# Kernel optimization log

Measured on AMD Instinct MI355X. Metric: run time of the kernel, lower is better.

## Reference

```python
import jax, jax.numpy as jnp
import numpy as np
import math

B_SZ, L, D_MODEL = 2, 2048, 1024
D_STATE, D_CONV, EXPAND = 16, 4, 2
D_INNER = EXPAND * D_MODEL
DT_RANK = math.ceil(D_MODEL / 16)


def setup_inputs() -> dict:
    key = jax.random.key(0)
    ks = jax.random.split(key, 9)
    s = 0.02
    x = jax.random.normal(ks[0], (B_SZ, L, D_MODEL), jnp.float32)
    W_in = jax.random.normal(ks[1], (D_MODEL, 2 * D_INNER), jnp.float32) * s
    conv_w = jax.random.normal(ks[2], (D_INNER, D_CONV), jnp.float32) * 0.1
    conv_b = jax.random.normal(ks[3], (D_INNER,), jnp.float32) * s
    W_xproj = jax.random.normal(ks[4], (D_INNER, DT_RANK + 2 * D_STATE), jnp.float32) * s
    W_dt = jax.random.normal(ks[5], (DT_RANK, D_INNER), jnp.float32) * s
    # dt bias init so softplus(bias) is log-uniform in [dt_min, dt_max]
    dt_min, dt_max = 0.001, 0.1
    dt = jnp.exp(jax.random.uniform(ks[6], (D_INNER,)) * (math.log(dt_max) - math.log(dt_min)) + math.log(dt_min))
    dt = jnp.maximum(dt, 1e-4)
    b_dt = dt + jnp.log(-jnp.expm1(-dt))
    A_log = jnp.log(jnp.broadcast_to(jnp.arange(1, D_STATE + 1, dtype=jnp.float32), (D_INNER, D_STATE)))
    D = jnp.ones((D_INNER,), jnp.float32)
    W_out = jax.random.normal(ks[7], (D_INNER, D_MODEL), jnp.float32) * s
    return {"x": x, "W_in": W_in, "conv_w": conv_w, "conv_b": conv_b,
            "W_xproj": W_xproj, "W_dt": W_dt, "b_dt": b_dt,
            "A_log": A_log, "D": D, "W_out": W_out}


def _silu(v):
    return v * jax.nn.sigmoid(v)


def _mamba_fwd(x, W_in, conv_w, conv_b, W_xproj, W_dt, b_dt, A_log, D, W_out):
    B, Ls, _ = x.shape
    xz = x @ W_in                         # (B, L, 2*d_inner)
    xb, z = jnp.split(xz, 2, axis=-1)
    # causal depthwise conv1d (pad left d_conv-1, truncate to L)
    xp = jnp.pad(xb, ((0, 0), (D_CONV - 1, 0), (0, 0)))
    conv = conv_b
    acc = jnp.zeros_like(xb)
    for k in range(D_CONV):
        acc = acc + xp[:, k:k + Ls, :] * conv_w[:, k]
    xb = _silu(acc + conv_b)
    # input-dependent dt, B, C
    proj = xb @ W_xproj                   # (B, L, dt_rank + 2*d_state)
    dt_in = proj[..., :DT_RANK]
    Bm = proj[..., DT_RANK:DT_RANK + D_STATE]   # (B, L, d_state)
    Cm = proj[..., DT_RANK + D_STATE:]          # (B, L, d_state)
    dt = jax.nn.softplus(dt_in @ W_dt + b_dt)   # (B, L, d_inner)
    A = -jnp.exp(A_log)                         # (d_inner, d_state)

    def step(h, inp):
        x_t, dt_t, B_t, C_t = inp               # (B,d_inner),(B,d_inner),(B,s),(B,s)
        dA = jnp.exp(dt_t[:, :, None] * A)      # (B, d_inner, d_state)
        h = dA * h + (dt_t[:, :, None] * B_t[:, None, :]) * x_t[:, :, None]
        y_t = jnp.einsum('bds,bs->bd', h, C_t)
        return h, y_t

    h0 = jnp.zeros((B, D_INNER, D_STATE), xb.dtype)
    xs = (xb.swapaxes(0, 1), dt.swapaxes(0, 1), Bm.swapaxes(0, 1), Cm.swapaxes(0, 1))
    _, ys = jax.lax.scan(step, h0, xs)          # (L, B, d_inner)
    y = ys.swapaxes(0, 1) + D * xb
    y = y * _silu(z)
    return y @ W_out                            # (B, L, d_model)


def reference(x, W_in, conv_w, conv_b, W_xproj, W_dt, b_dt, A_log, D, W_out):
    return _mamba_fwd(x, W_in, conv_w, conv_b, W_xproj, W_dt, b_dt, A_log, D, W_out)
```

## Files before the change

kernel.cpp:

```cpp
#include <hip/hip_runtime.h>
#include <hip/hip_bf16.h>
#include <math.h>

#define BSZ 2
#define LSEQ 2048
#define DMODEL 1024
#define DSTATE 16
#define DCONV 4
#define DINNER 2048
#define DTRANK 64
#define NPROJ (DTRANK + 2 * DSTATE)
#define NC 32
#define LC 64
#define KS 4
#define KCH (DINNER / KS)
#define TT 8

using short8 = __attribute__((ext_vector_type(8))) short;
using f32x4 = __attribute__((ext_vector_type(4))) float;
using u16x4 = __attribute__((ext_vector_type(4))) unsigned short;

__device__ __forceinline__ float silu_f(float v) {
    return v / (1.f + expf(-v));
}
__device__ __forceinline__ float softplus_f(float v) {
    return fmaxf(v, 0.f) + log1pf(expf(-fabsf(v)));
}
__device__ __forceinline__ unsigned short f2bf(float f) {
    unsigned u = __builtin_bit_cast(unsigned, f);
    u += 0x7fffu + ((u >> 16) & 1u);
    return (unsigned short)(u >> 16);
}
__device__ __forceinline__ float bf2f(unsigned short u) {
    unsigned x = ((unsigned)u) << 16;
    return __builtin_bit_cast(float, x);
}

__device__ __forceinline__ void gld_lds16(const unsigned short* g, unsigned short* l) {
    __builtin_amdgcn_global_load_lds(
        (const __attribute__((address_space(1))) unsigned int*)g,
        (__attribute__((address_space(3))) unsigned int*)l, 16, 0, 0);
}

__device__ __forceinline__ int xcd_swz(int wg, int nwg) {
    return (wg & 7) * (nwg >> 3) + (wg >> 3);
}

__global__ __launch_bounds__(256) void f32_to_bf16_kernel(
    const float* __restrict__ in, unsigned short* __restrict__ out, int n4) {
    int i = blockIdx.x * 256 + threadIdx.x;
    if (i >= n4) return;
    float4 v = reinterpret_cast<const float4*>(in)[i];
    u16x4 o = {f2bf(v.x), f2bf(v.y), f2bf(v.z), f2bf(v.w)};
    reinterpret_cast<u16x4*>(out)[i] = o;
}

__global__ __launch_bounds__(256) void transpose_bf16_kernel(
    const float* __restrict__ in, unsigned short* __restrict__ out, int R, int Cc) {
    __shared__ float t[32][33];
    const int tx = threadIdx.x & 31, ty = threadIdx.x >> 5;
    const int c0 = blockIdx.x * 32, r0 = blockIdx.y * 32;
    for (int i = ty; i < 32; i += 8)
        t[i][tx] = in[(size_t)(r0 + i) * Cc + c0 + tx];
    __syncthreads();
    for (int i = ty; i < 32; i += 8)
        out[(size_t)(c0 + i) * R + r0 + tx] = f2bf(t[tx][i]);
}

template <int EPI, typename CT>
__global__ __launch_bounds__(512) void gemm256(
    const unsigned short* __restrict__ A, const unsigned short* __restrict__ Bt,
    CT* __restrict__ C, CT* __restrict__ C2, int M, int N, int K) {
    extern __shared__ __align__(16) unsigned short lds[];
    unsigned short* As = lds;
    unsigned short* Bs = lds + 3 * 8192;
    const int tid = threadIdx.x;
    const int lane = tid & 63;
    const int w = tid >> 6;
    const int wm = w >> 2, wn = w & 3;
    const int nwg = gridDim.x * gridDim.y;
    const int wg = xcd_swz(blockIdx.y * gridDim.x + blockIdx.x, nwg);
    const int m0 = (wg / gridDim.x) * 256, n0 = (wg % gridDim.x) * 256;
    const int fr = lane & 15, kg = lane >> 4;
    const int kswz = ((kg ^ ((fr >> 1) & 3)) << 3);
    const int srow = tid >> 2;
    const int cs8 = (((tid & 3) ^ ((tid >> 3) & 3)) << 3);
    const int dst = tid * 8;
    const int nt = K / 32;

    f32x4 acc[8][4];
#pragma unroll
    for (int m = 0; m < 8; m++)
#pragma unroll
        for (int n = 0; n < 4; n++) acc[m][n] = (f32x4){0.f, 0.f, 0.f, 0.f};

#define STAGE_A(t)                                                               \
    {                                                                            \
        const int _b = (t) % 3, _k = (t) * 32;                                   \
        gld_lds16(&A[(size_t)(m0 + srow) * K + _k + cs8], &As[_b * 8192 + dst]); \
        gld_lds16(&A[(size_t)(m0 + 128 + srow) * K + _k + cs8],                  \
                  &As[_b * 8192 + dst + 4096]);                                  \
    }
#define STAGE_B(t)                                                               \
    {                                                                            \
        const int _b = (t) % 3, _k = (t) * 32;                                   \
        gld_lds16(&Bt[(size_t)(n0 + srow) * K + _k + cs8], &Bs[_b * 8192 + dst]);\
        gld_lds16(&Bt[(size_t)(n0 + 128 + srow) * K + _k + cs8],                 \
                  &Bs[_b * 8192 + dst + 4096]);                                  \
    }

    STAGE_A(0); STAGE_B(0); STAGE_A(1); STAGE_B(1);
    asm volatile("s_waitcnt vmcnt(4)" ::: "memory");
    __builtin_amdgcn_s_barrier();

    short8 bfr[4];
    for (int t = 0; t < nt; t++) {
        const int buf = t % 3;
        short8 afr[4];
#pragma unroll
        for (int q = 0; q < 4; q++)
            afr[q] = *reinterpret_cast<const short8*>(
                &As[buf * 8192 + (wm * 128 + q * 16 + fr) * 32 + kswz]);
#pragma unroll
        for (int q = 0; q < 4; q++)
            bfr[q] = *reinterpret_cast<const short8*>(
                &Bs[buf * 8192 + (wn * 64 + q * 16 + fr) * 32 + kswz]);
        if (t + 2 < nt) STAGE_A(t + 2);
        __builtin_amdgcn_s_barrier();
        asm volatile("s_waitcnt lgkmcnt(0)" ::: "memory");
        __builtin_amdgcn_sched_barrier(0);
        __builtin_amdgcn_s_setprio(1);
#pragma unroll
        for (int m = 0; m < 4; m++)
#pragma unroll
            for (int n = 0; n < 4; n++)
                acc[m][n] = __builtin_amdgcn_mfma_f32_16x16x32_bf16(
                    afr[m], bfr[n], acc[m][n], 0, 0, 0);
        __builtin_amdgcn_s_setprio(0);
        __builtin_amdgcn_s_barrier();
#pragma unroll
        for (int q = 0; q < 4; q++)
            afr[q] = *reinterpret_cast<const short8*>(
                &As[buf * 8192 + (wm * 128 + 64 + q * 16 + fr) * 32 + kswz]);
        if (t + 2 < nt) STAGE_B(t + 2);
        if (t + 1 < nt) {
            if (t + 2 < nt)
                asm volatile("s_waitcnt vmcnt(4)" ::: "memory");
            else
                asm volatile("s_waitcnt vmcnt(0)" ::: "memory");
        }
        __builtin_amdgcn_s_barrier();
        asm volatile("s_waitcnt lgkmcnt(0)" ::: "memory");
        __builtin_amdgcn_sched_barrier(0);
        __builtin_amdgcn_s_setprio(1);
#pragma unroll
        for (int m = 0; m < 4; m++)
#pragma unroll
            for (int n = 0; n < 4; n++)
                acc[4 + m][n] = __builtin_amdgcn_mfma_f32_16x16x32_bf16(
                    afr[m], bfr[n], acc[4 + m][n], 0, 0, 0);
        __builtin_amdgcn_s_setprio(0);
        __builtin_amdgcn_s_barrier();
    }
#undef STAGE_A
#undef STAGE_B

    const int g4 = kg * 4;
#pragma unroll
    for (int m = 0; m < 8; m++)
#pragma unroll
        for (int n = 0; n < 4; n++)
#pragma unroll
            for (int j = 0; j < 4; j++) {
                int mm = m0 + wm * 128 + m * 16 + g4 + j;
                int nn = n0 + wn * 64 + n * 16 + fr;
                float v = acc[m][n][j];
                if (EPI == 1) {
                    if (nn < DINNER)
                        C[(size_t)mm * DINNER + nn] = f2bf(v);
                    else
                        C2[(size_t)mm * DINNER + (nn - DINNER)] = f2bf(silu_f(v));
                } else {
                    if constexpr (sizeof(CT) == 2)
                        C[(size_t)mm * N + nn] = f2bf(v);
                    else
                        C[(size_t)mm * N + nn] = v;
                }
            }
}

template <int EPI, typename CT>
__global__ __launch_bounds__(256) void gemm_mfma(
    const unsigned short* __restrict__ A, const unsigned short* __restrict__ Bt,
    CT* __restrict__ C, int M, int N, int K) {
    __shared__ __align__(16) unsigned short As[2][4096];
    __shared__ __align__(16) unsigned short Bs[2][4096];
    const int tid = threadIdx.x;
    const int lane = tid & 63;
    const int wid = tid >> 6;
    const int wr = wid >> 1, wc = wid & 1;
    const int nwg = gridDim.x * gridDim.y;
    const int wg = xcd_swz(blockIdx.y * gridDim.x + blockIdx.x, nwg);
    const int m0 = (wg / gridDim.x) * 128, n0 = (wg % gridDim.x) * 128;

    const int r0 = tid >> 2;
    const int r1 = r0 + 64;
    const int d0 = tid * 8;
    const int d1 = d0 + 2048;
    const int cs8 = (((tid & 3) ^ ((tid >> 3) & 3)) << 3);

    f32x4 acc[4][4];
#pragma unroll
    for (int m = 0; m < 4; m++)
#pragma unroll
        for (int n = 0; n < 4; n++) acc[m][n] = (f32x4){0.f, 0.f, 0.f, 0.f};

    const int fr = lane & 15;
    const int kg = lane >> 4;
    const int kswz = ((kg ^ ((fr >> 1) & 3)) << 3);
    const int nt = K / 32;

    gld_lds16(&A[(size_t)(m0 + r0) * K + cs8], &As[0][d0]);
    gld_lds16(&A[(size_t)(m0 + r1) * K + cs8], &As[0][d1]);
    gld_lds16(&Bt[(size_t)(n0 + r0) * K + cs8], &Bs[0][d0]);
    gld_lds16(&Bt[(size_t)(n0 + r1) * K + cs8], &Bs[0][d1]);
    __syncthreads();

    int cur = 0;
    for (int t = 0; t < nt; t++) {
        if (t + 1 < nt) {
            const int k0 = (t + 1) * 32;
            gld_lds16(&A[(size_t)(m0 + r0) * K + k0 + cs8], &As[cur ^ 1][d0]);
            gld_lds16(&A[(size_t)(m0 + r1) * K + k0 + cs8], &As[cur ^ 1][d1]);
            gld_lds16(&Bt[(size_t)(n0 + r0) * K + k0 + cs8], &Bs[cur ^ 1][d0]);
            gld_lds16(&Bt[(size_t)(n0 + r1) * K + k0 + cs8], &Bs[cur ^ 1][d1]);
        }
        short8 a[4], b[4];
#pragma unroll
        for (int m = 0; m < 4; m++)
            a[m] = *reinterpret_cast<const short8*>(
                &As[cur][(wr * 64 + m * 16 + fr) * 32 + kswz]);
#pragma unroll
        for (int n = 0; n < 4; n++)
            b[n] = *reinterpret_cast<const short8*>(
                &Bs[cur][(wc * 64 + n * 16 + fr) * 32 + kswz]);
#pragma unroll
        for (int m = 0; m < 4; m++)
#pragma unroll
            for (int n = 0; n < 4; n++)
                acc[m][n] = __builtin_amdgcn_mfma_f32_16x16x32_bf16(
                    a[m], b[n], acc[m][n], 0, 0, 0);
        __syncthreads();
        cur ^= 1;
    }

    const int g4 = (lane >> 4) * 4;
#pragma unroll
    for (int m = 0; m < 4; m++)
#pragma unroll
        for (int n = 0; n < 4; n++)
#pragma unroll
            for (int j = 0; j < 4; j++) {
                int mm = m0 + wr * 64 + m * 16 + g4 + j;
                int nn = n0 + wc * 64 + n * 16 + fr;
                float v = acc[m][n][j];
                if constexpr (sizeof(CT) == 2)
                    C[(size_t)mm * N + nn] = f2bf(v);
                else
                    C[(size_t)mm * N + nn] = v;
            }
}

__global__ __launch_bounds__(256) void dt_gemm(
    const unsigned short* __restrict__ dtin,
    const unsigned short* __restrict__ WdtT,
    const float* __restrict__ bias,
    unsigned short* __restrict__ dtout) {
    const int lane = threadIdx.x & 63;
    const int wid = threadIdx.x >> 6;
    const int mt = wid >> 1, nh = wid & 1;
    const int m0 = blockIdx.x * 32;
    const int n0 = blockIdx.y * 128 + nh * 64;
    const int fr = lane & 15, kg = lane >> 4;

    f32x4 acc[4];
#pragma unroll
    for (int i = 0; i < 4; i++) acc[i] = (f32x4){0.f, 0.f, 0.f, 0.f};

#pragma unroll
    for (int step = 0; step < 2; step++) {
        short8 a = *reinterpret_cast<const short8*>(
            &dtin[(size_t)(m0 + mt * 16 + fr) * DTRANK + step * 32 + kg * 8]);
#pragma unroll
        for (int nt = 0; nt < 4; nt++) {
            short8 b = *reinterpret_cast<const short8*>(
                &WdtT[(size_t)(n0 + nt * 16 + fr) * DTRANK + step * 32 + kg * 8]);
            acc[nt] = __builtin_amdgcn_mfma_f32_16x16x32_bf16(a, b, acc[nt], 0, 0, 0);
        }
    }
    const int g4 = kg * 4;
#pragma unroll
    for (int nt = 0; nt < 4; nt++)
#pragma unroll
        for (int j = 0; j < 4; j++) {
            int m = m0 + mt * 16 + g4 + j;
            int n = n0 + nt * 16 + fr;
            dtout[(size_t)m * DINNER + n] = f2bf(softplus_f(acc[nt][j] + bias[n]));
        }
}

__global__ __launch_bounds__(256) void proj_splitk(
    const unsigned short* __restrict__ Abf,
    const unsigned short* __restrict__ WxT,
    float* __restrict__ pp) {
    const int lane = threadIdx.x & 63;
    const int wid = threadIdx.x >> 6;
    const int mt = wid >> 1;
    const int nh = wid & 1;
    const int m0 = blockIdx.x * 32;
    const int kc = blockIdx.y;
    const int fr = lane & 15;
    const int kg = lane >> 4;

    const size_t abase = (size_t)(m0 + mt * 16 + fr) * DINNER + kc * KCH + kg * 8;

    f32x4 acc[3];
#pragma unroll
    for (int i = 0; i < 3; i++) acc[i] = (f32x4){0.f, 0.f, 0.f, 0.f};

    for (int step = 0; step < KCH / 32; step++) {
        short8 a = *reinterpret_cast<const short8*>(&Abf[abase + step * 32]);
#pragma unroll
        for (int nt = 0; nt < 3; nt++) {
            int nrow = nh * 48 + nt * 16 + fr;
            short8 b = *reinterpret_cast<const short8*>(
                &WxT[(size_t)nrow * DINNER + kc * KCH + step * 32 + kg * 8]);
            acc[nt] = __builtin_amdgcn_mfma_f32_16x16x32_bf16(a, b, acc[nt], 0, 0, 0);
        }
    }
    const int g4 = (lane >> 4) * 4;
#pragma unroll
    for (int nt = 0; nt < 3; nt++)
#pragma unroll
        for (int j = 0; j < 4; j++) {
            int m = m0 + mt * 16 + g4 + j;
            int n = nh * 48 + nt * 16 + fr;
            pp[((size_t)kc * (BSZ * LSEQ) + m) * NPROJ + n] = acc[nt][j];
        }
}

__global__ __launch_bounds__(256) void proj_reduce(
    const float* __restrict__ pp, float* __restrict__ proj,
    unsigned short* __restrict__ dtin) {
    int i = blockIdx.x * 256 + threadIdx.x;
    if (i >= BSZ * LSEQ * NPROJ) return;
    float s = 0.f;
#pragma unroll
    for (int kc = 0; kc < KS; kc++)
        s += pp[(size_t)kc * BSZ * LSEQ * NPROJ + i];
    proj[i] = s;
    int m = i / NPROJ;
    int n = i - m * NPROJ;
    if (n < DTRANK) dtin[(size_t)m * DTRANK + n] = f2bf(s);
}

__global__ __launch_bounds__(256) void conv_silu_kernel(
    const unsigned short* __restrict__ xin, const float* __restrict__ w,
    const float* __restrict__ bconv, unsigned short* __restrict__ xout) {
    const int tid = threadIdx.x;
    const int d0 = tid * 8;
    const int bt0 = blockIdx.x * TT;
    const int tloc = bt0 & (LSEQ - 1);

    float wk0[8], wk1[8], wk2[8], wk3[8], bb[8];
#pragma unroll
    for (int q = 0; q < 8; q++) {
        float4 wv = *reinterpret_cast<const float4*>(&w[(d0 + q) * 4]);
        wk0[q] = wv.x; wk1[q] = wv.y; wk2[q] = wv.z; wk3[q] = wv.w;
    }
    {
        float4 b0 = *reinterpret_cast<const float4*>(&bconv[d0]);
        float4 b1 = *reinterpret_cast<const float4*>(&bconv[d0 + 4]);
        bb[0] = b0.x; bb[1] = b0.y; bb[2] = b0.z; bb[3] = b0.w;
        bb[4] = b1.x; bb[5] = b1.y; bb[6] = b1.z; bb[7] = b1.w;
    }

    float xm3[8], xm2[8], xm1[8];
    if (tloc >= 3) {
        short8 v3 = *reinterpret_cast<const short8*>(&xin[(size_t)(bt0 - 3) * DINNER + d0]);
        short8 v2 = *reinterpret_cast<const short8*>(&xin[(size_t)(bt0 - 2) * DINNER + d0]);
        short8 v1 = *reinterpret_cast<const short8*>(&xin[(size_t)(bt0 - 1) * DINNER + d0]);
#pragma unroll
        for (int q = 0; q < 8; q++) {
            xm3[q] = bf2f((unsigned short)v3[q]);
            xm2[q] = bf2f((unsigned short)v2[q]);
            xm1[q] = bf2f((unsigned short)v1[q]);
        }
    } else {
#pragma unroll
        for (int q = 0; q < 8; q++) { xm3[q] = 0.f; xm2[q] = 0.f; xm1[q] = 0.f; }
    }

#pragma unroll
    for (int i = 0; i < TT; i++) {
        short8 vc = *reinterpret_cast<const short8*>(&xin[(size_t)(bt0 + i) * DINNER + d0]);
        float xc[8];
        short8 o;
#pragma unroll
        for (int q = 0; q < 8; q++) {
            xc[q] = bf2f((unsigned short)vc[q]);
            float a = bb[q];
            a = fmaf(wk0[q], xm3[q], a);
            a = fmaf(wk1[q], xm2[q], a);
            a = fmaf(wk2[q], xm1[q], a);
            a = fmaf(wk3[q], xc[q], a);
            o[q] = (short)f2bf(silu_f(a));
        }
        *reinterpret_cast<short8*>(&xout[(size_t)(bt0 + i) * DINNER + d0]) = o;
#pragma unroll
        for (int q = 0; q < 8; q++) { xm3[q] = xm2[q]; xm2[q] = xm1[q]; xm1[q] = xc[q]; }
    }
}

__global__ __launch_bounds__(256) void scan_pass1(
    const unsigned short* __restrict__ xb, const unsigned short* __restrict__ dt,
    const float* __restrict__ proj, const float* __restrict__ A_log,
    float* __restrict__ aprod, float* __restrict__ hend) {
    __shared__ float Bs[LC][DSTATE];
    const int tg = blockIdx.x * 256 + threadIdx.x;
    const int d = tg & (DINNER - 1);
    const int bc = tg >> 11;
    const int c = bc & (NC - 1);
    const int b = bc >> 5;

    for (int idx = threadIdx.x; idx < LC * DSTATE; idx += 256) {
        int ti = idx >> 4, j = idx & 15;
        Bs[ti][j] = proj[(size_t)(b * LSEQ + c * LC + ti) * NPROJ + DTRANK + j];
    }
    __syncthreads();

    float Av[DSTATE], h[DSTATE], ap[DSTATE];
#pragma unroll
    for (int s = 0; s < DSTATE; s++) {
        Av[s] = -expf(A_log[d * DSTATE + s]);
        h[s] = 0.f;
        ap[s] = 1.f;
    }

    for (int i = 0; i < LC; i++) {
        size_t base = (size_t)(b * LSEQ + c * LC + i) * DINNER + d;
        float dtv = bf2f(dt[base]);
        float xv = bf2f(xb[base]);
        float dx = dtv * xv;
#pragma unroll
        for (int s = 0; s < DSTATE; s++) {
            float dA = __expf(dtv * Av[s]);
            ap[s] *= dA;
            h[s] = fmaf(dA, h[s], dx * Bs[i][s]);
        }
    }

    size_t o = ((size_t)bc * DINNER + d) * DSTATE;
#pragma unroll
    for (int q = 0; q < 4; q++) {
        *reinterpret_cast<float4*>(&aprod[o + q * 4]) =
            make_float4(ap[4 * q], ap[4 * q + 1], ap[4 * q + 2], ap[4 * q + 3]);
        *reinterpret_cast<float4*>(&hend[o + q * 4]) =
            make_float4(h[4 * q], h[4 * q + 1], h[4 * q + 2], h[4 * q + 3]);
    }
}

__global__ __launch_bounds__(256) void scan_pass2(
    float* __restrict__ aprod, const float* __restrict__ hend) {
    const int tg = blockIdx.x * 256 + threadIdx.x;
    const int s = tg & (DSTATE - 1);
    const int d = (tg >> 4) & (DINNER - 1);
    const int b = tg >> 15;
    float h = 0.f;
    for (int c = 0; c < NC; c++) {
        size_t o = ((size_t)((b * NC + c) * DINNER) + d) * DSTATE + s;
        float a = aprod[o];
        float e = hend[o];
        aprod[o] = h;
        h = fmaf(a, h, e);
    }
}

__global__ __launch_bounds__(256) void scan_pass3(
    const unsigned short* __restrict__ xb, const unsigned short* __restrict__ dt,
    const float* __restrict__ proj, const float* __restrict__ hstart,
    const float* __restrict__ A_log, const float* __restrict__ Dp,
    const unsigned short* __restrict__ sz, unsigned short* __restrict__ ybf) {
    __shared__ float Bs[LC][DSTATE];
    __shared__ float Cs[LC][DSTATE];
    const int tg = blockIdx.x * 256 + threadIdx.x;
    const int d = tg & (DINNER - 1);
    const int bc = tg >> 11;
    const int c = bc & (NC - 1);
    const int b = bc >> 5;

    for (int idx = threadIdx.x; idx < LC * 2 * DSTATE; idx += 256) {
        int ti = idx >> 5, j = idx & 31;
        float v = proj[(size_t)(b * LSEQ + c * LC + ti) * NPROJ + DTRANK + j];
        if (j < DSTATE) Bs[ti][j] = v;
        else            Cs[ti][j - DSTATE] = v;
    }
    __syncthreads();

    float Av[DSTATE], h[DSTATE];
    size_t o = ((size_t)bc * DINNER + d) * DSTATE;
#pragma unroll
    for (int q = 0; q < 4; q++) {
        float4 hv = *reinterpret_cast<const float4*>(&hstart[o + q * 4]);
        h[4 * q] = hv.x; h[4 * q + 1] = hv.y; h[4 * q + 2] = hv.z; h[4 * q + 3] = hv.w;
    }
#pragma unroll
    for (int s = 0; s < DSTATE; s++)
        Av[s] = -expf(A_log[d * DSTATE + s]);
    const float Dd = Dp[d];

    for (int i = 0; i < LC; i++) {
        size_t base = (size_t)(b * LSEQ + c * LC + i) * DINNER + d;
        float dtv = bf2f(dt[base]);
        float xv = bf2f(xb[base]);
        float szv = bf2f(sz[base]);
        float dx = dtv * xv;
        float p = 0.f;
#pragma unroll
        for (int s = 0; s < DSTATE; s++) {
            float dA = __expf(dtv * Av[s]);
            h[s] = fmaf(dA, h[s], dx * Bs[i][s]);
            p = fmaf(h[s], Cs[i][s], p);
        }
        ybf[base] = f2bf((p + Dd * xv) * szv);
    }
}

extern "C" void kernel_launch(void* const* d_in, const int* in_sizes, int n_in,
                              void* d_out, int out_size, void* d_ws,
                              size_t ws_size, hipStream_t stream) {
    const float* x = (const float*)d_in[0];
    const float* W_in = (const float*)d_in[1];
    const float* conv_w = (const float*)d_in[2];
    const float* conv_b = (const float*)d_in[3];
    const float* W_xproj = (const float*)d_in[4];
    const float* W_dt = (const float*)d_in[5];
    const float* b_dt = (const float*)d_in[6];
    const float* A_log = (const float*)d_in[7];
    const float* Dp = (const float*)d_in[8];
    const float* W_out = (const float*)d_in[9];
    float* out = (float*)d_out;

    char* ws = (char*)d_ws;
    const size_t MB = 1u << 20;
    float* pp    = (float*)(ws);
    float* aprod = (float*)(ws);
    float* hend  = (float*)(ws + 8 * MB);
    unsigned short* xbpre_bf = (unsigned short*)(ws + 16 * MB);
    unsigned short* ybf      = (unsigned short*)(ws + 16 * MB);
    unsigned short* sz_bf    = (unsigned short*)(ws + 32 * MB);
    unsigned short* xb_bf    = (unsigned short*)(ws + 48 * MB);
    unsigned short* dt_bf    = (unsigned short*)(ws + 64 * MB);
    float* projbuf           = (float*)(ws + 88 * MB);
    unsigned short* dtin_bf  = (unsigned short*)(ws + 90 * MB);
    unsigned short* xbf      = (unsigned short*)(ws + 91 * MB);
    unsigned short* WinT     = (unsigned short*)(ws + 99 * MB);
    unsigned short* WoutT    = (unsigned short*)(ws + 107 * MB);
    unsigned short* WxT      = (unsigned short*)(ws + 111 * MB);
    unsigned short* WdtT     = (unsigned short*)(ws + 112 * MB);

    const int M = BSZ * LSEQ;
    dim3 blk(256);

    f32_to_bf16_kernel<<<dim3((M * DMODEL / 4 + 255) / 256), blk, 0, stream>>>(
        x, xbf, M * DMODEL / 4);
    transpose_bf16_kernel<<<dim3(2 * DINNER / 32, DMODEL / 32), blk, 0, stream>>>(
        W_in, WinT, DMODEL, 2 * DINNER);
    transpose_bf16_kernel<<<dim3(DMODEL / 32, DINNER / 32), blk, 0, stream>>>(
        W_out, WoutT, DINNER, DMODEL);
    transpose_bf16_kernel<<<dim3(NPROJ / 32, DINNER / 32), blk, 0, stream>>>(
        W_xproj, WxT, DINNER, NPROJ);
    transpose_bf16_kernel<<<dim3(DINNER / 32, DTRANK / 32), blk, 0, stream>>>(
        W_dt, WdtT, DTRANK, DINNER);

    gemm256<1, unsigned short><<<dim3((2 * DINNER) / 256, M / 256), dim3(512),
                                 98304, stream>>>(
        xbf, WinT, xbpre_bf, sz_bf, M, 2 * DINNER, DMODEL);

    conv_silu_kernel<<<dim3(M / TT), blk, 0, stream>>>(
        xbpre_bf, conv_w, conv_b, xb_bf);

    proj_splitk<<<dim3(M / 32, KS), blk, 0, stream>>>(xb_bf, WxT, pp);
    proj_reduce<<<dim3((M * NPROJ) / 256), blk, 0, stream>>>(pp, projbuf, dtin_bf);

    dt_gemm<<<dim3(M / 32, DINNER / 128), blk, 0, stream>>>(
        dtin_bf, WdtT, b_dt, dt_bf);

    const int nthreads1 = BSZ * NC * DINNER;
    scan_pass1<<<dim3(nthreads1 / 256), blk, 0, stream>>>(
        xb_bf, dt_bf, projbuf, A_log, aprod, hend);
    const int nthreads2 = BSZ * DINNER * DSTATE;
    scan_pass2<<<dim3(nthreads2 / 256), blk, 0, stream>>>(aprod, hend);
    scan_pass3<<<dim3(nthreads1 / 256), blk, 0, stream>>>(
        xb_bf, dt_bf, projbuf, aprod, A_log, Dp, sz_bf, ybf);

    gemm_mfma<0, float><<<dim3(DMODEL / 128, M / 128), blk, 0, stream>>>(
        ybf, WoutT, out, M, DMODEL, DINNER);
}
```

Measured before the change: 270.1 us.

## Fuse prep kernels, retile input GEMM to 256x128, vectorize scan B/C loads

Result: faster. 259.3 us (-4.0%).

```diff
diff --git a/kernel.cpp b/kernel.cpp
--- a/kernel.cpp
+++ b/kernel.cpp
@@ -46,133 +46,108 @@
     return (wg & 7) * (nwg >> 3) + (wg >> 3);
 }
 
-__global__ __launch_bounds__(256) void f32_to_bf16_kernel(
-    const float* __restrict__ in, unsigned short* __restrict__ out, int n4) {
-    int i = blockIdx.x * 256 + threadIdx.x;
-    if (i >= n4) return;
-    float4 v = reinterpret_cast<const float4*>(in)[i];
-    u16x4 o = {f2bf(v.x), f2bf(v.y), f2bf(v.z), f2bf(v.w)};
-    reinterpret_cast<u16x4*>(out)[i] = o;
-}
-
-__global__ __launch_bounds__(256) void transpose_bf16_kernel(
-    const float* __restrict__ in, unsigned short* __restrict__ out, int R, int Cc) {
+__global__ __launch_bounds__(256) void prep_kernel(
+    const float* __restrict__ x, const float* __restrict__ W_in,
+    const float* __restrict__ W_out, const float* __restrict__ W_xproj,
+    const float* __restrict__ W_dt,
+    unsigned short* __restrict__ xbf, unsigned short* __restrict__ WinT,
+    unsigned short* __restrict__ WoutT, unsigned short* __restrict__ WxT,
+    unsigned short* __restrict__ WdtT) {
+    int bid = blockIdx.x;
+    if (bid < 4096) {
+        int i = bid * 256 + threadIdx.x;
+        float4 v = reinterpret_cast<const float4*>(x)[i];
+        u16x4 o = {f2bf(v.x), f2bf(v.y), f2bf(v.z), f2bf(v.w)};
+        reinterpret_cast<u16x4*>(xbf)[i] = o;
+        return;
+    }
+    bid -= 4096;
+    const float* in;
+    unsigned short* outp;
+    int R, Cc, gx;
+    if (bid < 4096) { in = W_in; outp = WinT; R = 1024; Cc = 4096; gx = 128; }
+    else if ((bid -= 4096) < 2048) { in = W_out; outp = WoutT; R = 2048; Cc = 1024; gx = 32; }
+    else if ((bid -= 2048) < 192) { in = W_xproj; outp = WxT; R = 2048; Cc = 96; gx = 3; }
+    else { bid -= 192; in = W_dt; outp = WdtT; R = 64; Cc = 2048; gx = 64; }
+    const int bx = bid % gx, by = bid / gx;
     __shared__ float t[32][33];
     const int tx = threadIdx.x & 31, ty = threadIdx.x >> 5;
-    const int c0 = blockIdx.x * 32, r0 = blockIdx.y * 32;
+    const int c0 = bx * 32, r0 = by * 32;
     for (int i = ty; i < 32; i += 8)
         t[i][tx] = in[(size_t)(r0 + i) * Cc + c0 + tx];
     __syncthreads();
     for (int i = ty; i < 32; i += 8)
-        out[(size_t)(c0 + i) * R + r0 + tx] = f2bf(t[tx][i]);
+        outp[(size_t)(c0 + i) * R + r0 + tx] = f2bf(t[tx][i]);
 }
 
 template <int EPI, typename CT>
-__global__ __launch_bounds__(512) void gemm256(
+__global__ __launch_bounds__(512, 4) void gemm_bm256(
     const unsigned short* __restrict__ A, const unsigned short* __restrict__ Bt,
     CT* __restrict__ C, CT* __restrict__ C2, int M, int N, int K) {
-    extern __shared__ __align__(16) unsigned short lds[];
-    unsigned short* As = lds;
-    unsigned short* Bs = lds + 3 * 8192;
+    __shared__ __align__(16) unsigned short As[2][8192];
+    __shared__ __align__(16) unsigned short Bs[2][4096];
     const int tid = threadIdx.x;
     const int lane = tid & 63;
-    const int w = tid >> 6;
-    const int wm = w >> 2, wn = w & 3;
+    const int w8 = tid >> 6;
+    const int wm = w8 >> 1, wn = w8 & 1;
     const int nwg = gridDim.x * gridDim.y;
     const int wg = xcd_swz(blockIdx.y * gridDim.x + blockIdx.x, nwg);
-    const int m0 = (wg / gridDim.x) * 256, n0 = (wg % gridDim.x) * 256;
+    const int m0 = (wg / gridDim.x) * 256, n0 = (wg % gridDim.x) * 128;
     const int fr = lane & 15, kg = lane >> 4;
     const int kswz = ((kg ^ ((fr >> 1) & 3)) << 3);
-    const int srow = tid >> 2;
+    const int r0 = tid >> 2;
+    const int d0 = tid * 8;
     const int cs8 = (((tid & 3) ^ ((tid >> 3) & 3)) << 3);
-    const int dst = tid * 8;
     const int nt = K / 32;
 
-    f32x4 acc[8][4];
-#pragma unroll
-    for (int m = 0; m < 8; m++)
+    f32x4 acc[4][4];
+#pragma unroll
+    for (int m = 0; m < 4; m++)
 #pragma unroll
         for (int n = 0; n < 4; n++) acc[m][n] = (f32x4){0.f, 0.f, 0.f, 0.f};
 
-#define STAGE_A(t)                                                               \
+#define STAGE(buf, k0)                                                           \
     {                                                                            \
-        const int _b = (t) % 3, _k = (t) * 32;                                   \
-        gld_lds16(&A[(size_t)(m0 + srow) * K + _k + cs8], &As[_b * 8192 + dst]); \
-        gld_lds16(&A[(size_t)(m0 + 128 + srow) * K + _k + cs8],                  \
-                  &As[_b * 8192 + dst + 4096]);                                  \
-    }
-#define STAGE_B(t)                                                               \
-    {                                                                            \
-        const int _b = (t) % 3, _k = (t) * 32;                                   \
-        gld_lds16(&Bt[(size_t)(n0 + srow) * K + _k + cs8], &Bs[_b * 8192 + dst]);\
-        gld_lds16(&Bt[(size_t)(n0 + 128 + srow) * K + _k + cs8],                 \
-                  &Bs[_b * 8192 + dst + 4096]);                                  \
-    }
-
-    STAGE_A(0); STAGE_B(0); STAGE_A(1); STAGE_B(1);
-    asm volatile("s_waitcnt vmcnt(4)" ::: "memory");
-    __builtin_amdgcn_s_barrier();
-
-    short8 bfr[4];
+        gld_lds16(&A[(size_t)(m0 + r0) * K + (k0) + cs8], &As[buf][d0]);         \
+        gld_lds16(&A[(size_t)(m0 + 128 + r0) * K + (k0) + cs8],                  \
+                  &As[buf][d0 + 4096]);                                          \
+        gld_lds16(&Bt[(size_t)(n0 + r0) * K + (k0) + cs8], &Bs[buf][d0]);        \
+    }
+
+    STAGE(0, 0);
+    __syncthreads();
+
+    int cur = 0;
     for (int t = 0; t < nt; t++) {
-        const int buf = t % 3;
-        short8 afr[4];
-#pragma unroll
-        for (int q = 0; q < 4; q++)
-            afr[q] = *reinterpret_cast<const short8*>(
-                &As[buf * 8192 + (wm * 128 + q * 16 + fr) * 32 + kswz]);
-#pragma unroll
-        for (int q = 0; q < 4; q++)
-            bfr[q] = *reinterpret_cast<const short8*>(
-                &Bs[buf * 8192 + (wn * 64 + q * 16 + fr) * 32 + kswz]);
-        if (t + 2 < nt) STAGE_A(t + 2);
-        __builtin_amdgcn_s_barrier();
-        asm volatile("s_waitcnt lgkmcnt(0)" ::: "memory");
-        __builtin_amdgcn_sched_barrier(0);
-        __builtin_amdgcn_s_setprio(1);
+        if (t + 1 < nt) STAGE(cur ^ 1, (t + 1) * 32);
+        short8 a[4], b[4];
+#pragma unroll
+        for (int m = 0; m < 4; m++)
+            a[m] = *reinterpret_cast<const short8*>(
+                &As[cur][(wm * 64 + m * 16 + fr) * 32 + kswz]);
+#pragma unroll
+        for (int n = 0; n < 4; n++)
+            b[n] = *reinterpret_cast<const short8*>(
+                &Bs[cur][(wn * 64 + n * 16 + fr) * 32 + kswz]);
 #pragma unroll
         for (int m = 0; m < 4; m++)
 #pragma unroll
             for (int n = 0; n < 4; n++)
                 acc[m][n] = __builtin_amdgcn_mfma_f32_16x16x32_bf16(
-                    afr[m], bfr[n], acc[m][n], 0, 0, 0);
-        __builtin_amdgcn_s_setprio(0);
-        __builtin_amdgcn_s_barrier();
-#pragma unroll
-        for (int q = 0; q < 4; q++)
-            afr[q] = *reinterpret_cast<const short8*>(
-                &As[buf * 8192 + (wm * 128 + 64 + q * 16 + fr) * 32 + kswz]);
-        if (t + 2 < nt) STAGE_B(t + 2);
-        if (t + 1 < nt) {
-            if (t + 2 < nt)
-                asm volatile("s_waitcnt vmcnt(4)" ::: "memory");
-            else
-                asm volatile("s_waitcnt vmcnt(0)" ::: "memory");
-        }
-        __builtin_amdgcn_s_barrier();
-        asm volatile("s_waitcnt lgkmcnt(0)" ::: "memory");
-        __builtin_amdgcn_sched_barrier(0);
-        __builtin_amdgcn_s_setprio(1);
-#pragma unroll
-        for (int m = 0; m < 4; m++)
-#pragma unroll
-            for (int n = 0; n < 4; n++)
-                acc[4 + m][n] = __builtin_amdgcn_mfma_f32_16x16x32_bf16(
-                    afr[m], bfr[n], acc[4 + m][n], 0, 0, 0);
-        __builtin_amdgcn_s_setprio(0);
-        __builtin_amdgcn_s_barrier();
-    }
-#undef STAGE_A
-#undef STAGE_B
+                    a[m], b[n], acc[m][n], 0, 0, 0);
+        __syncthreads();
+        cur ^= 1;
+    }
+#undef STAGE
 
     const int g4 = kg * 4;
 #pragma unroll
-    for (int m = 0; m < 8; m++)
+    for (int m = 0; m < 4; m++)
 #pragma unroll
         for (int n = 0; n < 4; n++)
 #pragma unroll
             for (int j = 0; j < 4; j++) {
-                int mm = m0 + wm * 128 + m * 16 + g4 + j;
+                int mm = m0 + wm * 64 + m * 16 + g4 + j;
                 int nn = n0 + wn * 64 + n * 16 + fr;
                 float v = acc[m][n][j];
                 if (EPI == 1) {
@@ -426,7 +401,7 @@
     const unsigned short* __restrict__ xb, const unsigned short* __restrict__ dt,
     const float* __restrict__ proj, const float* __restrict__ A_log,
     float* __restrict__ aprod, float* __restrict__ hend) {
-    __shared__ float Bs[LC][DSTATE];
+    __shared__ __align__(16) float Bsh[LC][DSTATE];
     const int tg = blockIdx.x * 256 + threadIdx.x;
     const int d = tg & (DINNER - 1);
     const int bc = tg >> 11;
@@ -435,7 +410,7 @@
 
     for (int idx = threadIdx.x; idx < LC * DSTATE; idx += 256) {
         int ti = idx >> 4, j = idx & 15;
-        Bs[ti][j] = proj[(size_t)(b * LSEQ + c * LC + ti) * NPROJ + DTRANK + j];
+        Bsh[ti][j] = proj[(size_t)(b * LSEQ + c * LC + ti) * NPROJ + DTRANK + j];
     }
     __syncthreads();
 
@@ -452,11 +427,16 @@
         float dtv = bf2f(dt[base]);
         float xv = bf2f(xb[base]);
         float dx = dtv * xv;
+        float Bv[DSTATE];
+        *reinterpret_cast<float4*>(&Bv[0])  = *reinterpret_cast<const float4*>(&Bsh[i][0]);
+        *reinterpret_cast<float4*>(&Bv[4])  = *reinterpret_cast<const float4*>(&Bsh[i][4]);
+        *reinterpret_cast<float4*>(&Bv[8])  = *reinterpret_cast<const float4*>(&Bsh[i][8]);
+        *reinterpret_cast<float4*>(&Bv[12]) = *reinterpret_cast<const float4*>(&Bsh[i][12]);
 #pragma unroll
         for (int s = 0; s < DSTATE; s++) {
             float dA = __expf(dtv * Av[s]);
             ap[s] *= dA;
-            h[s] = fmaf(dA, h[s], dx * Bs[i][s]);
+            h[s] = fmaf(dA, h[s], dx * Bv[s]);
         }
     }
 
@@ -491,8 +471,8 @@
     const float* __restrict__ proj, const float* __restrict__ hstart,
     const float* __restrict__ A_log, const float* __restrict__ Dp,
     const unsigned short* __restrict__ sz, unsigned short* __restrict__ ybf) {
-    __shared__ float Bs[LC][DSTATE];
-    __shared__ float Cs[LC][DSTATE];
+    __shared__ __align__(16) float Bsh[LC][DSTATE];
+    __shared__ __align__(16) float Csh[LC][DSTATE];
     const int tg = blockIdx.x * 256 + threadIdx.x;
     const int d = tg & (DINNER - 1);
     const int bc = tg >> 11;
@@ -502,8 +482,8 @@
     for (int idx = threadIdx.x; idx < LC * 2 * DSTATE; idx += 256) {
         int ti = idx >> 5, j = idx & 31;
         float v = proj[(size_t)(b * LSEQ + c * LC + ti) * NPROJ + DTRANK + j];
-        if (j < DSTATE) Bs[ti][j] = v;
-        else            Cs[ti][j - DSTATE] = v;
+        if (j < DSTATE) Bsh[ti][j] = v;
+        else            Csh[ti][j - DSTATE] = v;
     }
     __syncthreads();
 
@@ -525,12 +505,21 @@
         float xv = bf2f(xb[base]);
         float szv = bf2f(sz[base]);
         float dx = dtv * xv;
+        float Bv[DSTATE], Cv[DSTATE];
+        *reinterpret_cast<float4*>(&Bv[0])  = *reinterpret_cast<const float4*>(&Bsh[i][0]);
+        *reinterpret_cast<float4*>(&Bv[4])  = *reinterpret_cast<const float4*>(&Bsh[i][4]);
+        *reinterpret_cast<float4*>(&Bv[8])  = *reinterpret_cast<const float4*>(&Bsh[i][8]);
+        *reinterpret_cast<float4*>(&Bv[12]) = *reinterpret_cast<const float4*>(&Bsh[i][12]);
+        *reinterpret_cast<float4*>(&Cv[0])  = *reinterpret_cast<const float4*>(&Csh[i][0]);
+        *reinterpret_cast<float4*>(&Cv[4])  = *reinterpret_cast<const float4*>(&Csh[i][4]);
+        *reinterpret_cast<float4*>(&Cv[8])  = *reinterpret_cast<const float4*>(&Csh[i][8]);
+        *reinterpret_cast<float4*>(&Cv[12]) = *reinterpret_cast<const float4*>(&Csh[i][12]);
         float p = 0.f;
 #pragma unroll
         for (int s = 0; s < DSTATE; s++) {
             float dA = __expf(dtv * Av[s]);
-            h[s] = fmaf(dA, h[s], dx * Bs[i][s]);
-            p = fmaf(h[s], Cs[i][s], p);
+            h[s] = fmaf(dA, h[s], dx * Bv[s]);
+            p = fmaf(h[s], Cv[s], p);
         }
         ybf[base] = f2bf((p + Dd * xv) * szv);
     }
@@ -572,19 +561,11 @@
     const int M = BSZ * LSEQ;
     dim3 blk(256);
 
-    f32_to_bf16_kernel<<<dim3((M * DMODEL / 4 + 255) / 256), blk, 0, stream>>>(
-        x, xbf, M * DMODEL / 4);
-    transpose_bf16_kernel<<<dim3(2 * DINNER / 32, DMODEL / 32), blk, 0, stream>>>(
-        W_in, WinT, DMODEL, 2 * DINNER);
-    transpose_bf16_kernel<<<dim3(DMODEL / 32, DINNER / 32), blk, 0, stream>>>(
-        W_out, WoutT, DINNER, DMODEL);
-    transpose_bf16_kernel<<<dim3(NPROJ / 32, DINNER / 32), blk, 0, stream>>>(
-        W_xproj, WxT, DINNER, NPROJ);
-    transpose_bf16_kernel<<<dim3(DINNER / 32, DTRANK / 32), blk, 0, stream>>>(
-        W_dt, WdtT, DTRANK, DINNER);
-
-    gemm256<1, unsigned short><<<dim3((2 * DINNER) / 256, M / 256), dim3(512),
-                                 98304, stream>>>(
+    prep_kernel<<<dim3(4096 + 4096 + 2048 + 192 + 128), blk, 0, stream>>>(
+        x, W_in, W_out, W_xproj, W_dt, xbf, WinT, WoutT, WxT, WdtT);
+
+    gemm_bm256<1, unsigned short><<<dim3((2 * DINNER) / 128, M / 256), dim3(512),
+                                    0, stream>>>(
         xbf, WinT, xbpre_bf, sz_bf, M, 2 * DINNER, DMODEL);
 
     conv_silu_kernel<<<dim3(M / TT), blk, 0, stream>>>(
```
